# Performance work log

Measured on AMD Instinct MI355X. Metric: run time of the kernel, lower is better.

The kernel has to match this reference:

```python
import jax, jax.numpy as jnp
import numpy as np

# --- SLAYER params (nmnistNet.yaml) ---
THETA = 10.0
TS = 1.0
TAU_REF = 1.0
SCALE_REF = 2.0
T_SAMPLE = 300
B = 8

def _alpha_kernel(tau, mult, t_sample, ts, eps=0.01):
    vals = []
    t = 0.0
    while t < t_sample:
        v = mult * t / tau * np.exp(1.0 - t / tau)
        if abs(v) < eps and t > tau:
            break
        vals.append(v)
        t += ts
    return np.asarray(vals, np.float32)

# refractory kernel: alpha kernel with mult = -scaleRef*theta (slayer._calculateRefKernel)
REF_KERNEL = _alpha_kernel(TAU_REF, -SCALE_REF * THETA, T_SAMPLE, TS)
NREF = REF_KERNEL.shape[0]  # 11 for these params; REF_KERNEL[0] == 0


def spike(u):
    """slayerCuda.getSpikes: per-neuron sequential threshold recurrence over time.
    u: [..., T] membrane potential. On spike at t, REF_KERNEL is accumulated
    into u[t:t+NREF]; spike amplitude is 1/Ts."""
    uT = jnp.moveaxis(u, -1, 0)  # [T, ...]
    refk = jnp.asarray(REF_KERNEL[1:]).reshape((NREF - 1,) + (1,) * (u.ndim - 1))
    buf0 = jnp.zeros((NREF - 1,) + uT.shape[1:], u.dtype)  # pending refractory

    def step(buf, u_t):
        u_mod = u_t + buf[0]
        ev = (u_mod >= THETA).astype(u.dtype)
        buf = jnp.concatenate([buf[1:], jnp.zeros_like(buf[:1])], axis=0) + ev[None] * refk
        return buf, ev / TS

    _, s = jax.lax.scan(step, buf0, uT)
    return jnp.moveaxis(s, 0, -1)


def conv2d_t(x, w, pad):
    """slayer.conv: Conv3d with kernel (k,k,1) == per-timestep 2D conv.
    x: [B,C,H,W,T], w: [O,I,kh,kw]."""
    b, c, h, wd, t = x.shape
    xb = jnp.moveaxis(x, -1, 1).reshape(b * t, c, h, wd)
    y = jax.lax.conv_general_dilated(xb, w, (1, 1), [(pad, pad), (pad, pad)],
                                     dimension_numbers=('NCHW', 'OIHW', 'NCHW'))
    o, ho, wo = y.shape[1], y.shape[2], y.shape[3]
    return jnp.moveaxis(y.reshape(b, t, o, ho, wo), 1, -1)


def sum_pool2(x):
    """slayer.pool(2): fixed-weight (1.1*theta) 2x2/stride-2 sum over H,W per channel."""
    y = jax.lax.reduce_window(x, 0.0, jax.lax.add, (1, 1, 2, 2, 1), (1, 1, 2, 2, 1), 'VALID')
    return 1.1 * THETA * y


def setup_inputs():
    key = jax.random.key(0)
    k0, k1, k2, k3, k4 = jax.random.split(key, 5)
    spikeInput = (jax.random.uniform(k0, (B, 2, 34, 34, T_SAMPLE)) < 0.1).astype(jnp.float32) / TS
    # conv weights: kaiming-uniform bound * 100 (the __init__ scales conv weights by 100)
    w1 = jax.random.uniform(k1, (16, 2, 5, 5), minval=-14.1, maxval=14.1, dtype=jnp.float32)
    w2 = jax.random.uniform(k2, (32, 16, 3, 3), minval=-8.3, maxval=8.3, dtype=jnp.float32)
    w3 = jax.random.uniform(k3, (64, 32, 3, 3), minval=-5.9, maxval=5.9, dtype=jnp.float32)
    wfc = jax.random.uniform(k4, (10, 64, 8, 8), minval=-0.5, maxval=0.5, dtype=jnp.float32)
    return {"spikeInput": spikeInput, "w1": w1, "w2": w2, "w3": w3, "wfc": wfc}


def reference(spikeInput, w1, w2, w3, wfc):
    s1 = spike(conv2d_t(spikeInput, w1, 1))  # [B,16,32,32,T]
    s2 = spike(sum_pool2(s1))                # [B,16,16,16,T]
    s3 = spike(conv2d_t(s2, w2, 1))          # [B,32,16,16,T]
    s4 = spike(sum_pool2(s3))                # [B,32,8,8,T]
    s5 = spike(conv2d_t(s4, w3, 1))          # [B,64,8,8,T]
    # dense((8,8,64),10): Conv3d(64,10,(8,8,1)) == full-spatial contraction
    u = jnp.einsum('bchwt,ochw->bot', s5, wfc)[:, :, None, None, :]
    return spike(u)                          # [B,10,1,1,T]
```

## Files before the change

### kernel.cpp

```cpp
#include <hip/hip_runtime.h>
#include <hip/hip_bf16.h>
#include <cmath>

#define T_SAMPLE 300
#define NCHUNK 75

typedef __attribute__((ext_vector_type(8))) short short8;
typedef __attribute__((ext_vector_type(4))) float f32x4;

struct RefK { float v[10]; };

__device__ __forceinline__ unsigned char spike_step(float u, float* buf, const RefK& rk) {
    const float um = u + buf[0];
    const bool fire = um >= 10.0f;
    const float ev = fire ? 1.0f : 0.0f;
#pragma unroll
    for (int r = 0; r < 9; ++r) buf[r] = fmaf(ev, rk.v[r], buf[r + 1]);
    buf[9] = ev * rk.v[9];
    return fire ? (unsigned char)1 : (unsigned char)0;
}

__device__ __forceinline__ short8 bytes_to_bf16x8(uint2 w8) {
    union { uint4 u; short8 s8; } cv;
    cv.u.x = (w8.x & 0xFFu) * 0x3F80u | ((((w8.x >> 8) & 0xFFu) * 0x3F80u) << 16);
    cv.u.y = ((w8.x >> 16) & 0xFFu) * 0x3F80u | ((((w8.x >> 24) & 0xFFu) * 0x3F80u) << 16);
    cv.u.z = (w8.y & 0xFFu) * 0x3F80u | ((((w8.y >> 8) & 0xFFu) * 0x3F80u) << 16);
    cv.u.w = ((w8.y >> 16) & 0xFFu) * 0x3F80u | ((((w8.y >> 24) & 0xFFu) * 0x3F80u) << 16);
    return cv.s8;
}

__device__ __forceinline__ unsigned short bf16_split_sel(float w, int s) {
    __hip_bfloat16 hb = __float2bfloat16(w);
    const float hf = __bfloat162float(hb);
    __hip_bfloat16 mb = __float2bfloat16(w - hf);
    const float mf = __bfloat162float(mb);
    __hip_bfloat16 lb = __float2bfloat16(w - hf - mf);
    __hip_bfloat16 sel = (s == 0) ? hb : ((s == 1) ? mb : lb);
    return *(unsigned short*)&sel;
}

__global__ __launch_bounds__(256) void transpose_in_k(
    const float* __restrict__ In, unsigned int* __restrict__ X)
{
    __shared__ unsigned int lds[16 * NCHUNK];
    const int blk = blockIdx.x;
    const int tn = threadIdx.x >> 4;
    const int tq = threadIdx.x & 15;
    const size_t n = (size_t)blk * 16 + tn;
#pragma unroll
    for (int p = 0; p < 5; ++p) {
        const int ch = p * 16 + tq;
        if (ch < NCHUNK) {
            const float4 v = *(const float4*)(In + n * T_SAMPLE + ch * 4);
            unsigned int u = (v.x != 0.f ? 1u : 0u) | (v.y != 0.f ? 0x100u : 0u) |
                             (v.z != 0.f ? 0x10000u : 0u) | (v.w != 0.f ? 0x1000000u : 0u);
            lds[tn * NCHUNK + ch] = u;
        }
    }
    __syncthreads();
    for (int idx = threadIdx.x; idx < 16 * NCHUNK; idx += 256) {
        const int ch = idx >> 4, t2 = idx & 15;
        X[(size_t)ch * 18496 + blk * 16 + t2] = lds[t2 * NCHUNK + ch];
    }
}

__global__ __launch_bounds__(256) void prep_w1_k(
    const float* __restrict__ w1, unsigned short* __restrict__ Wr1)
{
    const int g = blockIdx.x * 256 + threadIdx.x;
    const int j = g & 7;
    const int lane = (g >> 3) & 63;
    const int ks = (g >> 9) & 3;
    const int s = g >> 11;
    const int q = lane >> 4;
    const int oc = lane & 15;
    const int kg = ks * 32 + q * 8 + j;
    const int slot = kg >> 2, c = kg & 1;
    const int dy = slot / 6, dx = slot % 6;
    const float w = (dy < 5 && dx < 5) ? w1[((oc * 2 + c) * 5 + dy) * 5 + dx] * 0.5f : 0.f;
    Wr1[g] = bf16_split_sel(w, s);
}

__global__ __launch_bounds__(256) void prep_w3_k(
    const float* __restrict__ w3, unsigned short* __restrict__ Wr)
{
    const int g = blockIdx.x * 256 + threadIdx.x;
    const int j = g & 7;
    const int lane = (g >> 3) & 63;
    const int mt = (g >> 9) & 3;
    const int rest = g >> 11;
    const int ks = rest % 9;
    const int s = rest / 9;
    const int oc = mt * 16 + (lane & 15);
    const int ic = (lane >> 4) * 8 + j;
    Wr[g] = bf16_split_sel(w3[(oc * 32 + ic) * 9 + ks], s);
}

__global__ __launch_bounds__(256) void prep_w2_k(
    const float* __restrict__ w2, unsigned short* __restrict__ Wr2)
{
    const int g = blockIdx.x * 256 + threadIdx.x;
    const int j = g & 7;
    const int lane = (g >> 3) & 63;
    const int mt = (g >> 9) & 1;
    const int rest = g >> 10;
    const int kp = rest % 5;
    const int s = rest / 5;
    const int q = lane >> 4;
    const int oc = mt * 16 + (lane & 15);
    const int tap = kp * 2 + (q >> 1);
    const int ic = (q & 1) * 8 + j;
    const float w = (tap <= 8) ? w2[(oc * 16 + ic) * 9 + tap] : 0.f;
    Wr2[g] = bf16_split_sel(w, s);
}

__global__ __launch_bounds__(256) void conv1_mfma_k(
    const unsigned int* __restrict__ Xu, const unsigned short* __restrict__ Wr1,
    float4* __restrict__ U, int b0, int nbl)
{
    __shared__ __align__(16) unsigned int pad[768];
    const int tc = blockIdx.x;
    const int tile = blockIdx.y;
    const int ty = tile >> 2, tx = tile & 3;
    const int bl = blockIdx.z;
    const int b = b0 + bl;
    const int tid = threadIdx.x;
    const int wv = tid >> 6, lane = tid & 63;
    const int q = lane >> 4, n = lane & 15;
    const int PLANE_U = nbl * 16384;

    for (int i = tid; i < 768; i += 256) pad[i] = 0u;
    __syncthreads();
    const unsigned int* xb = Xu + (size_t)tc * 18496;
    if (tid < 192) {
        const int r = tid >> 4, col = tid & 15;
        const int y = ty * 8 + r - 1, x = tx * 8 + col - 1;
        unsigned int w0 = 0u, w1v = 0u;
        if ((unsigned)y < 34u && (unsigned)x < 34u) {
            w0 = xb[((b * 2 + 0) * 34 + y) * 34 + x];
            w1v = xb[((b * 2 + 1) * 34 + y) * 34 + x];
        }
#pragma unroll
        for (int t = 0; t < 4; ++t) {
            const unsigned int b0b = (w0 >> (8 * t)) & 0xFFu;
            const unsigned int b1b = (w1v >> (8 * t)) & 0xFFu;
            pad[(t * 12 + r) * 16 + col] = b0b | (b1b << 8) | (b0b << 16) | (b1b << 24);
        }
    }
    __syncthreads();

    const int pixel = wv * 16 + n;
    const int py0 = pixel >> 3, px0 = pixel & 7;

    short8 Af[12];
#pragma unroll
    for (int s = 0; s < 3; ++s)
#pragma unroll
        for (int ks = 0; ks < 4; ++ks)
            Af[s * 4 + ks] = *(const short8*)(Wr1 + (((s * 4 + ks) * 64 + lane) * 8));

    f32x4 acc[4];
#pragma unroll
    for (int t = 0; t < 4; ++t) acc[t] = (f32x4){0.f, 0.f, 0.f, 0.f};

#pragma unroll
    for (int ks = 0; ks < 4; ++ks) {
        const int slotA = ks * 8 + q * 2, slotB = slotA + 1;
        const int dyA = slotA / 6, dxA = slotA - dyA * 6;
        const int dyB = slotB / 6, dxB = slotB - dyB * 6;
        const int trA = min(py0 + dyA, 11), trB = min(py0 + dyB, 11);
        const int tcA = px0 + dxA, tcB = px0 + dxB;
#pragma unroll
        for (int t = 0; t < 4; ++t) {
            uint2 w8;
            w8.x = pad[(t * 12 + trA) * 16 + tcA];
            w8.y = pad[(t * 12 + trB) * 16 + tcB];
            const short8 Bf = bytes_to_bf16x8(w8);
#pragma unroll
            for (int s = 0; s < 3; ++s)
                acc[t] = __builtin_amdgcn_mfma_f32_16x16x32_bf16(
                    Af[s * 4 + ks], Bf, acc[t], 0, 0, 0);
        }
    }

    const int y = ty * 8 + py0, x = tx * 8 + px0;
    const size_t ub = (size_t)tc * PLANE_U;
#pragma unroll
    for (int rr = 0; rr < 4; ++rr) {
        const int oc = q * 4 + rr;
        const int nb = (bl * 16 + oc) * 1024 + y * 32 + x;
        U[ub + nb] = make_float4(acc[0][rr], acc[1][rr], acc[2][rr], acc[3][rr]);
    }
}

__global__ __launch_bounds__(256) void conv2_mfma_k(
    const unsigned int* __restrict__ s2u, const unsigned short* __restrict__ Wr2,
    float4* __restrict__ U, int b0, int nbl)
{
    __shared__ __align__(16) unsigned char pad[4 * 18 * 18 * 16];
    const int tc = blockIdx.x;
    const int bl = blockIdx.z;
    const int b = b0 + bl;
    const int tid = threadIdx.x;
    const int wv = tid >> 6, lane = tid & 63;
    const int q = lane >> 4, n = lane & 15;
    const int PLANE_U = nbl * 8192;

    unsigned int* lp = (unsigned int*)pad;
    for (int i = tid; i < 5184; i += 256) lp[i] = 0u;
    __syncthreads();
    const unsigned int* sb = s2u + (size_t)tc * 32768 + b * 4096;
    for (int e = tid; e < 4096; e += 256) {
        const unsigned int v = sb[e];
        const int c = e >> 8, pix = e & 255;
        const int base = (((pix >> 4) + 1) * 18 + ((pix & 15) + 1)) * 16 + c;
        pad[base]         = (unsigned char)(v & 0xFFu);
        pad[5184 + base]  = (unsigned char)((v >> 8) & 0xFFu);
        pad[10368 + base] = (unsigned char)((v >> 16) & 0xFFu);
        pad[15552 + base] = (unsigned char)(v >> 24);
    }
    __syncthreads();

    for (int i = 0; i < 4; ++i) {
        const int r = wv * 4 + i;
        f32x4 acc[2][4];
#pragma unroll
        for (int mt = 0; mt < 2; ++mt)
#pragma unroll
            for (int t = 0; t < 4; ++t) acc[mt][t] = (f32x4){0.f, 0.f, 0.f, 0.f};

        for (int kp = 0; kp < 5; ++kp) {
            short8 Af[6];
#pragma unroll
            for (int s = 0; s < 3; ++s)
#pragma unroll
                for (int mt = 0; mt < 2; ++mt)
                    Af[s * 2 + mt] = *(const short8*)(Wr2 + ((((s * 5 + kp) * 2 + mt) * 64 + lane) * 8));
            int tap = kp * 2 + (q >> 1);
            if (tap > 8) tap = 8;
            const int dy = tap / 3, dx = tap % 3;
#pragma unroll
            for (int t = 0; t < 4; ++t) {
                const int off = ((t * 18 + r + dy) * 18 + (n + dx)) * 16 + (q & 1) * 8;
                const short8 Bf = bytes_to_bf16x8(*(const uint2*)(pad + off));
#pragma unroll
                for (int s = 0; s < 3; ++s)
#pragma unroll
                    for (int mt = 0; mt < 2; ++mt)
                        acc[mt][t] = __builtin_amdgcn_mfma_f32_16x16x32_bf16(
                            Af[s * 2 + mt], Bf, acc[mt][t], 0, 0, 0);
            }
        }

        const size_t ub = (size_t)tc * PLANE_U;
#pragma unroll
        for (int mt = 0; mt < 2; ++mt)
#pragma unroll
            for (int rr = 0; rr < 4; ++rr) {
                const int oc = mt * 16 + q * 4 + rr;
                const int nb = (bl * 32 + oc) * 256 + r * 16 + n;
                U[ub + nb] = make_float4(acc[mt][0][rr], acc[mt][1][rr], acc[mt][2][rr], acc[mt][3][rr]);
            }
    }
}

__global__ __launch_bounds__(256) void conv3_mfma_k(
    const unsigned int* __restrict__ s4u, const unsigned short* __restrict__ Wr,
    float4* __restrict__ U)
{
    __shared__ __align__(16) unsigned char pad[12800];
    const int tc = blockIdx.x;
    const int bl = blockIdx.z;
    const int tid = threadIdx.x;
    const int wv = tid >> 6, lane = tid & 63;
    const int q = lane >> 4, n = lane & 15;

    unsigned int* lp = (unsigned int*)pad;
    for (int i = tid; i < 3200; i += 256) lp[i] = 0u;
    __syncthreads();
    const unsigned int* sb = s4u + (size_t)tc * 16384 + bl * 2048;
    for (int e = tid; e < 2048; e += 256) {
        const unsigned int v = sb[e];
        const int c = e >> 6, pix = e & 63;
        const int base = (((pix >> 3) + 1) * 10 + ((pix & 7) + 1)) * 32 + c;
        pad[base]        = (unsigned char)(v & 0xFFu);
        pad[3200 + base] = (unsigned char)((v >> 8) & 0xFFu);
        pad[6400 + base] = (unsigned char)((v >> 16) & 0xFFu);
        pad[9600 + base] = (unsigned char)(v >> 24);
    }
    __syncthreads();

    const int pixel = wv * 16 + n;
    const int py0 = pixel >> 3, px0 = pixel & 7;

    f32x4 acc[4][4];
#pragma unroll
    for (int mt = 0; mt < 4; ++mt)
#pragma unroll
        for (int t = 0; t < 4; ++t) acc[mt][t] = (f32x4){0.f, 0.f, 0.f, 0.f};

    for (int ks = 0; ks < 9; ++ks) {
        const int dy = ks / 3, dx = ks % 3;
        short8 Af[12];
#pragma unroll
        for (int s = 0; s < 3; ++s)
#pragma unroll
            for (int mt = 0; mt < 4; ++mt)
                Af[s * 4 + mt] = *(const short8*)(Wr + ((((s * 9 + ks) * 4 + mt) * 64 + lane) * 8));
#pragma unroll
        for (int t = 0; t < 4; ++t) {
            const int off = ((t * 10 + py0 + dy) * 10 + (px0 + dx)) * 32 + q * 8;
            const short8 Bf = bytes_to_bf16x8(*(const uint2*)(pad + off));
#pragma unroll
            for (int s = 0; s < 3; ++s)
#pragma unroll
                for (int mt = 0; mt < 4; ++mt)
                    acc[mt][t] = __builtin_amdgcn_mfma_f32_16x16x32_bf16(
                        Af[s * 4 + mt], Bf, acc[mt][t], 0, 0, 0);
        }
    }

    const size_t ub = (size_t)tc * 32768 + (size_t)bl * 4096;
#pragma unroll
    for (int mt = 0; mt < 4; ++mt)
#pragma unroll
        for (int r = 0; r < 4; ++r) {
            const int oc = mt * 16 + q * 4 + r;
            const int nb = oc * 64 + wv * 16 + n;
            U[ub + nb] = make_float4(acc[mt][0][r], acc[mt][1][r], acc[mt][2][r], acc[mt][3][r]);
        }
}

__device__ __forceinline__ void spike_body(
    const float4* __restrict__ U, uchar4* __restrict__ S,
    int nneur, int sstride, int soff, const RefK& rk)
{
    const int n = blockIdx.x * 64 + threadIdx.x;
    const float4* up = U + n;
    uchar4* sp = S + soff + n;
    float buf[10];
#pragma unroll
    for (int r = 0; r < 10; ++r) buf[r] = 0.f;

    float4 ring[8];
#pragma unroll
    for (int r = 0; r < 8; ++r) ring[r] = up[(size_t)r * nneur];

#pragma unroll 8
    for (int ch = 0; ch < 72; ++ch) {
        const float4 cur = ring[ch & 7];
        const int pf = (ch + 8 < NCHUNK) ? ch + 8 : NCHUNK - 1;
        ring[ch & 7] = up[(size_t)pf * nneur];
        uchar4 o;
        o.x = spike_step(cur.x, buf, rk);
        o.y = spike_step(cur.y, buf, rk);
        o.z = spike_step(cur.z, buf, rk);
        o.w = spike_step(cur.w, buf, rk);
        sp[(size_t)ch * sstride] = o;
    }
#pragma unroll
    for (int ch = 72; ch < NCHUNK; ++ch) {
        const float4 cur = ring[ch & 7];
        uchar4 o;
        o.x = spike_step(cur.x, buf, rk);
        o.y = spike_step(cur.y, buf, rk);
        o.z = spike_step(cur.z, buf, rk);
        o.w = spike_step(cur.w, buf, rk);
        sp[(size_t)ch * sstride] = o;
    }
}

__global__ __launch_bounds__(64) void spike1_k(
    const float4* U, uchar4* S, int nneur, int sstride, int soff, RefK rk)
{ spike_body(U, S, nneur, sstride, soff, rk); }

__global__ __launch_bounds__(64) void spike2_k(
    const float4* U, uchar4* S, int nneur, int sstride, int soff, RefK rk)
{ spike_body(U, S, nneur, sstride, soff, rk); }

__global__ __launch_bounds__(64) void spike3_k(
    const float4* U, uchar4* S, int nneur, int sstride, int soff, RefK rk)
{ spike_body(U, S, nneur, sstride, soff, rk); }

__device__ __forceinline__ int bsum4(uint2 r0, uint2 r1, int k) {
    return (int)((r0.x >> (8 * k)) & 0xffu) + (int)((r0.y >> (8 * k)) & 0xffu)
         + (int)((r1.x >> (8 * k)) & 0xffu) + (int)((r1.y >> (8 * k)) & 0xffu);
}

template <int C, int H, int W>
__device__ __forceinline__ void pool_body(
    const uchar4* __restrict__ Sin, uchar4* __restrict__ Sout, const RefK& rk)
{
    constexpr int H2 = H / 2, W2 = W / 2;
    constexpr int SIN = 8 * C * H * W;
    constexpr int SOUT = 8 * C * H2 * W2;
    const int n = blockIdx.x * 64 + threadIdx.x;
    const int x = n % W2;
    const int y = (n / W2) % H2;
    const int c = (n / (W2 * H2)) % C;
    const int b = n / (W2 * H2 * C);
    const int base = (((b * C + c) * H + 2 * y) * W + 2 * x);
    uchar4* q = Sout + n;

    float buf[10];
#pragma unroll
    for (int r = 0; r < 10; ++r) buf[r] = 0.f;

    uint2 r0[8], r1[8];
#pragma unroll
    for (int r = 0; r < 8; ++r) {
        r0[r] = *(const uint2*)(Sin + (size_t)r * SIN + base);
        r1[r] = *(const uint2*)(Sin + (size_t)r * SIN + base + W);
    }

#pragma unroll 8
    for (int ch = 0; ch < 72; ++ch) {
        const uint2 a0 = r0[ch & 7], a1 = r1[ch & 7];
        const int pf = (ch + 8 < NCHUNK) ? ch + 8 : NCHUNK - 1;
        r0[ch & 7] = *(const uint2*)(Sin + (size_t)pf * SIN + base);
        r1[ch & 7] = *(const uint2*)(Sin + (size_t)pf * SIN + base + W);
        uchar4 o;
        o.x = spike_step(11.0f * (float)bsum4(a0, a1, 0), buf, rk);
        o.y = spike_step(11.0f * (float)bsum4(a0, a1, 1), buf, rk);
        o.z = spike_step(11.0f * (float)bsum4(a0, a1, 2), buf, rk);
        o.w = spike_step(11.0f * (float)bsum4(a0, a1, 3), buf, rk);
        q[(size_t)ch * SOUT] = o;
    }
#pragma unroll
    for (int ch = 72; ch < NCHUNK; ++ch) {
        const uint2 a0 = r0[ch & 7], a1 = r1[ch & 7];
        uchar4 o;
        o.x = spike_step(11.0f * (float)bsum4(a0, a1, 0), buf, rk);
        o.y = spike_step(11.0f * (float)bsum4(a0, a1, 1), buf, rk);
        o.z = spike_step(11.0f * (float)bsum4(a0, a1, 2), buf, rk);
        o.w = spike_step(11.0f * (float)bsum4(a0, a1, 3), buf, rk);
        q[(size_t)ch * SOUT] = o;
    }
}

__global__ __launch_bounds__(64) void pool2_k(
    const uchar4* Sin, uchar4* Sout, RefK rk) { pool_body<16, 32, 32>(Sin, Sout, rk); }
__global__ __launch_bounds__(64) void pool4_k(
    const uchar4* Sin, uchar4* Sout, RefK rk) { pool_body<32, 16, 16>(Sin, Sout, rk); }

__global__ __launch_bounds__(64) void dense_k(
    const uchar4* __restrict__ S5, const float* __restrict__ WFC,
    float4* __restrict__ U6)
{
    const int tc = blockIdx.x, o = blockIdx.y, b = blockIdx.z;
    const int lane = threadIdx.x;
    float a0 = 0.f, a1 = 0.f, a2 = 0.f, a3 = 0.f;
    const uchar4* sb = S5 + (size_t)tc * 32768 + b * 4096;
    const float* wb = WFC + o * 4096;
    for (int i = 0; i < 64; ++i) {
        const int site = i * 64 + lane;
        const uchar4 s = sb[site];
        const float w = wb[site];
        a0 = fmaf(w, (float)s.x, a0);
        a1 = fmaf(w, (float)s.y, a1);
        a2 = fmaf(w, (float)s.z, a2);
        a3 = fmaf(w, (float)s.w, a3);
    }
#pragma unroll
    for (int m = 1; m < 64; m <<= 1) {
        a0 += __shfl_xor(a0, m, 64);
        a1 += __shfl_xor(a1, m, 64);
        a2 += __shfl_xor(a2, m, 64);
        a3 += __shfl_xor(a3, m, 64);
    }
    if (lane == 0)
        U6[(size_t)tc * 80 + b * 10 + o] = make_float4(a0, a1, a2, a3);
}

__global__ __launch_bounds__(128) void spike6_k(
    const float4* __restrict__ U6, float* __restrict__ Out, RefK rk)
{
    const int n = threadIdx.x;
    if (n >= 80) return;
    const float4* up = U6 + n;
    float* op = Out + (size_t)n * T_SAMPLE;
    float buf[10];
#pragma unroll
    for (int r = 0; r < 10; ++r) buf[r] = 0.f;

    float4 ring[8];
#pragma unroll
    for (int r = 0; r < 8; ++r) ring[r] = up[(size_t)r * 80];

#pragma unroll 8
    for (int ch = 0; ch < 72; ++ch) {
        const float4 cur = ring[ch & 7];
        const int pf = (ch + 8 < NCHUNK) ? ch + 8 : NCHUNK - 1;
        ring[ch & 7] = up[(size_t)pf * 80];
        float4 o;
        o.x = (float)spike_step(cur.x, buf, rk);
        o.y = (float)spike_step(cur.y, buf, rk);
        o.z = (float)spike_step(cur.z, buf, rk);
        o.w = (float)spike_step(cur.w, buf, rk);
        *(float4*)(op + ch * 4) = o;
    }
#pragma unroll
    for (int ch = 72; ch < NCHUNK; ++ch) {
        const float4 cur = ring[ch & 7];
        float4 o;
        o.x = (float)spike_step(cur.x, buf, rk);
        o.y = (float)spike_step(cur.y, buf, rk);
        o.z = (float)spike_step(cur.z, buf, rk);
        o.w = (float)spike_step(cur.w, buf, rk);
        *(float4*)(op + ch * 4) = o;
    }
}

extern "C" void kernel_launch(void* const* d_in, const int* in_sizes, int n_in,
                              void* d_out, int out_size, void* d_ws, size_t ws_size,
                              hipStream_t stream)
{
    const float* spikeIn = (const float*)d_in[0];
    const float* w1 = (const float*)d_in[1];
    const float* w2 = (const float*)d_in[2];
    const float* w3 = (const float*)d_in[3];
    const float* wfc = (const float*)d_in[4];
    float* out = (float*)d_out;

    RefK rk;
    for (int t = 1; t <= 10; ++t)
        rk.v[t - 1] = (float)(-20.0 * (double)t * std::exp(1.0 - (double)t));

    const size_t A_BYTES = 39321600;
    const size_t B_BYTES = 9830400;
    const size_t U6_BYTES = 96000;
    const size_t U_HUGE = 157286400, U_BIG = 78643200, U_SMALL = 39321600;
    const size_t TAIL = A_BYTES + B_BYTES + U6_BYTES;
    const bool huge = ws_size >= U_HUGE + TAIL;
    const bool big = ws_size >= U_BIG + TAIL;
    const size_t U_BYTES = huge ? U_HUGE : (big ? U_BIG : U_SMALL);

    char* ws = (char*)d_ws;
    float4* U = (float4*)ws;
    uchar4* A = (uchar4*)(ws + U_BYTES);
    uchar4* Bb = (uchar4*)(ws + U_BYTES + A_BYTES);
    float4* U6 = (float4*)(ws + U_BYTES + A_BYTES + B_BYTES);
    unsigned short* Wr = (unsigned short*)(ws + U_BYTES + 20971520);
    unsigned short* Wr2 = (unsigned short*)(ws + U_BYTES + 20971520 + 131072);
    unsigned short* Wr1 = (unsigned short*)(ws + U_BYTES + A_BYTES + 5570560);

    uchar4* X = Bb;
    uchar4* s1 = A;
    uchar4* s2 = Bb;
    uchar4* s3 = A;
    uchar4* s4 = Bb;
    uchar4* s5 = A;

    transpose_in_k<<<18496 / 16, 256, 0, stream>>>(spikeIn, (unsigned int*)X);
    prep_w1_k<<<24, 256, 0, stream>>>(w1, Wr1);

    const int nbl1 = huge ? 8 : (big ? 4 : 2);
    for (int b0 = 0; b0 < 8; b0 += nbl1) {
        dim3 g1(NCHUNK, 16, nbl1);
        conv1_mfma_k<<<g1, 256, 0, stream>>>((const unsigned int*)X, Wr1, U, b0, nbl1);
        const int nn = nbl1 * 16384;
        spike1_k<<<nn / 64, 64, 0, stream>>>(U, s1, nn, 131072, b0 * 16384, rk);
    }
    pool2_k<<<32768 / 64, 64, 0, stream>>>(s1, s2, rk);
    prep_w2_k<<<60, 256, 0, stream>>>(w2, Wr2);
    prep_w3_k<<<216, 256, 0, stream>>>(w3, Wr);
    const int nbl2 = (huge || big) ? 8 : 4;
    for (int b0 = 0; b0 < 8; b0 += nbl2) {
        dim3 g2(NCHUNK, 1, nbl2);
        conv2_mfma_k<<<g2, 256, 0, stream>>>((const unsigned int*)s2, Wr2, U, b0, nbl2);
        const int nn = nbl2 * 8192;
        spike2_k<<<nn / 64, 64, 0, stream>>>(U, s3, nn, 65536, b0 * 8192, rk);
    }
    pool4_k<<<16384 / 64, 64, 0, stream>>>(s3, s4, rk);
    {
        dim3 g3(NCHUNK, 1, 8);
        conv3_mfma_k<<<g3, 256, 0, stream>>>((const unsigned int*)s4, Wr, U);
        spike3_k<<<32768 / 64, 64, 0, stream>>>(U, s5, 32768, 32768, 0, rk);
    }
    dim3 g6(NCHUNK, 10, 8);
    dense_k<<<g6, 64, 0, stream>>>(s5, wfc, U6);
    spike6_k<<<1, 128, 0, stream>>>(U6, out, rk);
}
```

Baseline: 287.8 us.

## Fuse conv1 with spike recurrence, iterating time chunks inside one kernel

Replaces the conv1 kernel and its separate spike pass with a fused kernel. Each 64-thread block owns a 2x8 pixel tile for one batch and loops over all 75 time chunks, carrying refractory state in registers and prefetching the next chunk into registers. This removes the large float membrane-potential buffer round trip through global memory. A new repack kernel pre-expands input bytes to bf16 pairs. The cost is a grid of only 512 small blocks running a serial time loop, which lowers parallelism and latency hiding.

```diff
diff --git a/kernel.cpp b/kernel.cpp
--- a/kernel.cpp
+++ b/kernel.cpp
@@ -61,6 +61,25 @@
     for (int idx = threadIdx.x; idx < 16 * NCHUNK; idx += 256) {
         const int ch = idx >> 4, t2 = idx & 15;
         X[(size_t)ch * 18496 + blk * 16 + t2] = lds[t2 * NCHUNK + ch];
+    }
+}
+
+__global__ __launch_bounds__(256) void repack1_k(
+    const unsigned int* __restrict__ X, uint2* __restrict__ X2)
+{
+    const int g = blockIdx.x * 256 + threadIdx.x;
+    if (g >= 693600) return;
+    const int yx = g % 1156;
+    const int rest = g / 1156;
+    const int b = rest & 7;
+    const int ch = rest >> 3;
+    const unsigned int w0 = X[(size_t)ch * 18496 + (b * 2 + 0) * 1156 + yx];
+    const unsigned int w1 = X[(size_t)ch * 18496 + (b * 2 + 1) * 1156 + yx];
+#pragma unroll
+    for (int t = 0; t < 4; ++t) {
+        const unsigned int u = ((w0 >> (8 * t)) & 0xFFu) * 0x3F80u
+                             | ((((w1 >> (8 * t)) & 0xFFu) * 0x3F80u) << 16);
+        X2[(((size_t)ch * 4 + t) * 8 + b) * 1156 + yx] = make_uint2(u, u);
     }
 }
 
@@ -114,43 +133,17 @@
     Wr2[g] = bf16_split_sel(w, s);
 }
 
-__global__ __launch_bounds__(256) void conv1_mfma_k(
-    const unsigned int* __restrict__ Xu, const unsigned short* __restrict__ Wr1,
-    float4* __restrict__ U, int b0, int nbl)
-{
-    __shared__ __align__(16) unsigned int pad[768];
-    const int tc = blockIdx.x;
-    const int tile = blockIdx.y;
-    const int ty = tile >> 2, tx = tile & 3;
-    const int bl = blockIdx.z;
-    const int b = b0 + bl;
-    const int tid = threadIdx.x;
-    const int wv = tid >> 6, lane = tid & 63;
+__global__ __launch_bounds__(64) void conv1s_mfma_k(
+    const uint2* __restrict__ X2, const unsigned short* __restrict__ Wr1,
+    uchar4* __restrict__ S1, RefK rk)
+{
+    __shared__ __align__(16) uint2 sh[288];
+    const int pg = blockIdx.x;
+    const int b = blockIdx.y;
+    const int ty = pg >> 2, tx = pg & 3;
+    const int lane = threadIdx.x;
     const int q = lane >> 4, n = lane & 15;
-    const int PLANE_U = nbl * 16384;
-
-    for (int i = tid; i < 768; i += 256) pad[i] = 0u;
-    __syncthreads();
-    const unsigned int* xb = Xu + (size_t)tc * 18496;
-    if (tid < 192) {
-        const int r = tid >> 4, col = tid & 15;
-        const int y = ty * 8 + r - 1, x = tx * 8 + col - 1;
-        unsigned int w0 = 0u, w1v = 0u;
-        if ((unsigned)y < 34u && (unsigned)x < 34u) {
-            w0 = xb[((b * 2 + 0) * 34 + y) * 34 + x];
-            w1v = xb[((b * 2 + 1) * 34 + y) * 34 + x];
-        }
-#pragma unroll
-        for (int t = 0; t < 4; ++t) {
-            const unsigned int b0b = (w0 >> (8 * t)) & 0xFFu;
-            const unsigned int b1b = (w1v >> (8 * t)) & 0xFFu;
-            pad[(t * 12 + r) * 16 + col] = b0b | (b1b << 8) | (b0b << 16) | (b1b << 24);
-        }
-    }
-    __syncthreads();
-
-    const int pixel = wv * 16 + n;
-    const int py0 = pixel >> 3, px0 = pixel & 7;
+    const int py0 = n >> 3, px0 = n & 7;
 
     short8 Af[12];
 #pragma unroll
@@ -159,37 +152,83 @@
         for (int ks = 0; ks < 4; ++ks)
             Af[s * 4 + ks] = *(const short8*)(Wr1 + (((s * 4 + ks) * 64 + lane) * 8));
 
-    f32x4 acc[4];
-#pragma unroll
-    for (int t = 0; t < 4; ++t) acc[t] = (f32x4){0.f, 0.f, 0.f, 0.f};
-
+    int lofs[5]; int gofs[5]; bool gval[5];
+#pragma unroll
+    for (int i = 0; i < 5; ++i) {
+        const int e = i * 64 + lane;
+        if (e < 288) {
+            const int t = e / 72, s = e - t * 72;
+            const int r = s / 12, cc = s - r * 12;
+            const int gy = ty * 2 - 1 + r, gx = tx * 8 - 1 + cc;
+            gval[i] = ((unsigned)gy < 34u) && ((unsigned)gx < 34u);
+            lofs[i] = e;
+            gofs[i] = (t * 8 + b) * 1156 + gy * 34 + gx;
+        } else { gval[i] = false; lofs[i] = -1; gofs[i] = 0; }
+    }
+
+    uint2 pf[5];
+#pragma unroll
+    for (int i = 0; i < 5; ++i) pf[i] = make_uint2(0u, 0u);
+#pragma unroll
+    for (int i = 0; i < 5; ++i) if (gval[i]) pf[i] = X2[gofs[i]];
+
+    int offA[4], offB[4];
 #pragma unroll
     for (int ks = 0; ks < 4; ++ks) {
-        const int slotA = ks * 8 + q * 2, slotB = slotA + 1;
-        const int dyA = slotA / 6, dxA = slotA - dyA * 6;
-        const int dyB = slotB / 6, dxB = slotB - dyB * 6;
-        const int trA = min(py0 + dyA, 11), trB = min(py0 + dyB, 11);
-        const int tcA = px0 + dxA, tcB = px0 + dxB;
-#pragma unroll
-        for (int t = 0; t < 4; ++t) {
-            uint2 w8;
-            w8.x = pad[(t * 12 + trA) * 16 + tcA];
-            w8.y = pad[(t * 12 + trB) * 16 + tcB];
-            const short8 Bf = bytes_to_bf16x8(w8);
-#pragma unroll
-            for (int s = 0; s < 3; ++s)
-                acc[t] = __builtin_amdgcn_mfma_f32_16x16x32_bf16(
-                    Af[s * 4 + ks], Bf, acc[t], 0, 0, 0);
+        const int sA = ks * 8 + q * 2, sB = sA + 1;
+        const int dyA = sA / 6, dxA = sA - dyA * 6;
+        const int dyB = sB / 6, dxB = sB - dyB * 6;
+        offA[ks] = min(py0 + dyA, 5) * 12 + min(px0 + dxA, 11);
+        offB[ks] = min(py0 + dyB, 5) * 12 + min(px0 + dxB, 11);
+    }
+
+    float buf[4][10];
+#pragma unroll
+    for (int rr = 0; rr < 4; ++rr)
+#pragma unroll
+        for (int r = 0; r < 10; ++r) buf[rr][r] = 0.f;
+
+    const int nb0 = (b * 16 + q * 4) * 1024 + (ty * 2 + py0) * 32 + tx * 8 + px0;
+
+    for (int ch = 0; ch < NCHUNK; ++ch) {
+        __syncthreads();
+#pragma unroll
+        for (int i = 0; i < 5; ++i) if (lofs[i] >= 0) sh[lofs[i]] = pf[i];
+        __syncthreads();
+
+        if (ch + 1 < NCHUNK) {
+            const uint2* src = X2 + (size_t)(ch + 1) * 36992;
+#pragma unroll
+            for (int i = 0; i < 5; ++i) if (gval[i]) pf[i] = src[gofs[i]];
         }
-    }
-
-    const int y = ty * 8 + py0, x = tx * 8 + px0;
-    const size_t ub = (size_t)tc * PLANE_U;
-#pragma unroll
-    for (int rr = 0; rr < 4; ++rr) {
-        const int oc = q * 4 + rr;
-        const int nb = (bl * 16 + oc) * 1024 + y * 32 + x;
-        U[ub + nb] = make_float4(acc[0][rr], acc[1][rr], acc[2][rr], acc[3][rr]);
+
+        f32x4 acc[4];
+#pragma unroll
+        for (int t = 0; t < 4; ++t) acc[t] = (f32x4){0.f, 0.f, 0.f, 0.f};
+
+#pragma unroll
+        for (int ks = 0; ks < 4; ++ks)
+#pragma unroll
+            for (int t = 0; t < 4; ++t) {
+                const uint2 a = sh[offA[ks] + t * 72];
+                const uint2 bq = sh[offB[ks] + t * 72];
+                union { uint4 u; short8 s8; } cv;
+                cv.u.x = a.x; cv.u.y = a.y; cv.u.z = bq.x; cv.u.w = bq.y;
+#pragma unroll
+                for (int s = 0; s < 3; ++s)
+                    acc[t] = __builtin_amdgcn_mfma_f32_16x16x32_bf16(
+                        Af[s * 4 + ks], cv.s8, acc[t], 0, 0, 0);
+            }
+
+#pragma unroll
+        for (int rr = 0; rr < 4; ++rr) {
+            uchar4 o;
+            o.x = spike_step(acc[0][rr], buf[rr], rk);
+            o.y = spike_step(acc[1][rr], buf[rr], rk);
+            o.z = spike_step(acc[2][rr], buf[rr], rk);
+            o.w = spike_step(acc[3][rr], buf[rr], rk);
+            S1[(size_t)ch * 131072 + nb0 + rr * 1024] = o;
+        }
     }
 }
 
@@ -369,10 +408,6 @@
         sp[(size_t)ch * sstride] = o;
     }
 }
-
-__global__ __launch_bounds__(64) void spike1_k(
-    const float4* U, uchar4* S, int nneur, int sstride, int soff, RefK rk)
-{ spike_body(U, S, nneur, sstride, soff, rk); }
 
 __global__ __launch_bounds__(64) void spike2_k(
     const float4* U, uchar4* S, int nneur, int sstride, int soff, RefK rk)
@@ -543,6 +578,7 @@
     unsigned short* Wr = (unsigned short*)(ws + U_BYTES + 20971520);
     unsigned short* Wr2 = (unsigned short*)(ws + U_BYTES + 20971520 + 131072);
     unsigned short* Wr1 = (unsigned short*)(ws + U_BYTES + A_BYTES + 5570560);
+    uint2* X2 = (uint2*)ws;
 
     uchar4* X = Bb;
     uchar4* s1 = A;
@@ -553,13 +589,11 @@
 
     transpose_in_k<<<18496 / 16, 256, 0, stream>>>(spikeIn, (unsigned int*)X);
     prep_w1_k<<<24, 256, 0, stream>>>(w1, Wr1);
-
-    const int nbl1 = huge ? 8 : (big ? 4 : 2);
-    for (int b0 = 0; b0 < 8; b0 += nbl1) {
-        dim3 g1(NCHUNK, 16, nbl1);
-        conv1_mfma_k<<<g1, 256, 0, stream>>>((const unsigned int*)X, Wr1, U, b0, nbl1);
-        const int nn = nbl1 * 16384;
-        spike1_k<<<nn / 64, 64, 0, stream>>>(U, s1, nn, 131072, b0 * 16384, rk);
+    repack1_k<<<2710, 256, 0, stream>>>((const unsigned int*)X, X2);
+
+    {
+        dim3 g1(64, 8);
+        conv1s_mfma_k<<<g1, 64, 0, stream>>>(X2, Wr1, s1, rk);
     }
     pool2_k<<<32768 / 64, 64, 0, stream>>>(s1, s2, rk);
     prep_w2_k<<<60, 256, 0, stream>>>(w2, Wr2);
```

New measurement: 394.3 us. +37.0%, slower.

## Split conv1/conv2 and spike stages into time phases with carried refractory state

Applied to the files above, without the earlier changes.

Rather than batching conv+spike over subsets of the batch, the conv1 and conv2 stages are now split along time into phases (5 of 15 chunks, 3 of 25 chunks), with all 8 batches per launch. The spike kernel saves its refractory buffer to a state array between phases and reloads it at the start of the next. This keeps the membrane-potential buffer smaller and more cache-resident, and gives every spike launch the full neuron count for better parallelism. The cost is extra state reads and writes and more kernel launches. The workspace-size branching is also removed.

```diff
diff --git a/kernel.cpp b/kernel.cpp
--- a/kernel.cpp
+++ b/kernel.cpp
@@ -116,22 +116,20 @@
 
 __global__ __launch_bounds__(256) void conv1_mfma_k(
     const unsigned int* __restrict__ Xu, const unsigned short* __restrict__ Wr1,
-    float4* __restrict__ U, int b0, int nbl)
+    float4* __restrict__ U, int c0)
 {
     __shared__ __align__(16) unsigned int pad[768];
-    const int tc = blockIdx.x;
+    const int tcl = blockIdx.x;
     const int tile = blockIdx.y;
     const int ty = tile >> 2, tx = tile & 3;
-    const int bl = blockIdx.z;
-    const int b = b0 + bl;
+    const int b = blockIdx.z;
     const int tid = threadIdx.x;
     const int wv = tid >> 6, lane = tid & 63;
     const int q = lane >> 4, n = lane & 15;
-    const int PLANE_U = nbl * 16384;
 
     for (int i = tid; i < 768; i += 256) pad[i] = 0u;
     __syncthreads();
-    const unsigned int* xb = Xu + (size_t)tc * 18496;
+    const unsigned int* xb = Xu + (size_t)(c0 + tcl) * 18496;
     if (tid < 192) {
         const int r = tid >> 4, col = tid & 15;
         const int y = ty * 8 + r - 1, x = tx * 8 + col - 1;
@@ -184,32 +182,30 @@
     }
 
     const int y = ty * 8 + py0, x = tx * 8 + px0;
-    const size_t ub = (size_t)tc * PLANE_U;
+    const size_t ub = (size_t)tcl * 131072;
 #pragma unroll
     for (int rr = 0; rr < 4; ++rr) {
         const int oc = q * 4 + rr;
-        const int nb = (bl * 16 + oc) * 1024 + y * 32 + x;
+        const int nb = (b * 16 + oc) * 1024 + y * 32 + x;
         U[ub + nb] = make_float4(acc[0][rr], acc[1][rr], acc[2][rr], acc[3][rr]);
     }
 }
 
 __global__ __launch_bounds__(256) void conv2_mfma_k(
     const unsigned int* __restrict__ s2u, const unsigned short* __restrict__ Wr2,
-    float4* __restrict__ U, int b0, int nbl)
+    float4* __restrict__ U, int c0)
 {
     __shared__ __align__(16) unsigned char pad[4 * 18 * 18 * 16];
-    const int tc = blockIdx.x;
-    const int bl = blockIdx.z;
-    const int b = b0 + bl;
+    const int tcl = blockIdx.x;
+    const int b = blockIdx.z;
     const int tid = threadIdx.x;
     const int wv = tid >> 6, lane = tid & 63;
     const int q = lane >> 4, n = lane & 15;
-    const int PLANE_U = nbl * 8192;
 
     unsigned int* lp = (unsigned int*)pad;
     for (int i = tid; i < 5184; i += 256) lp[i] = 0u;
     __syncthreads();
-    const unsigned int* sb = s2u + (size_t)tc * 32768 + b * 4096;
+    const unsigned int* sb = s2u + (size_t)(c0 + tcl) * 32768 + b * 4096;
     for (int e = tid; e < 4096; e += 256) {
         const unsigned int v = sb[e];
         const int c = e >> 8, pix = e & 255;
@@ -252,13 +248,13 @@
             }
         }
 
-        const size_t ub = (size_t)tc * PLANE_U;
+        const size_t ub = (size_t)tcl * 65536;
 #pragma unroll
         for (int mt = 0; mt < 2; ++mt)
 #pragma unroll
             for (int rr = 0; rr < 4; ++rr) {
                 const int oc = mt * 16 + q * 4 + rr;
-                const int nb = (bl * 32 + oc) * 256 + r * 16 + n;
+                const int nb = (b * 32 + oc) * 256 + r * 16 + n;
                 U[ub + nb] = make_float4(acc[mt][0][rr], acc[mt][1][rr], acc[mt][2][rr], acc[mt][3][rr]);
             }
     }
@@ -331,56 +327,55 @@
         }
 }
 
-__device__ __forceinline__ void spike_body(
+template <int TB>
+__global__ __launch_bounds__(64) void spike_phase_k(
     const float4* __restrict__ U, uchar4* __restrict__ S,
-    int nneur, int sstride, int soff, const RefK& rk)
+    float* __restrict__ St, int nneur, int c0, RefK rk)
 {
     const int n = blockIdx.x * 64 + threadIdx.x;
     const float4* up = U + n;
-    uchar4* sp = S + soff + n;
+    uchar4* sp = S + (size_t)c0 * nneur + n;
+
     float buf[10];
-#pragma unroll
-    for (int r = 0; r < 10; ++r) buf[r] = 0.f;
+    if (c0 == 0) {
+#pragma unroll
+        for (int r = 0; r < 10; ++r) buf[r] = 0.f;
+    } else {
+#pragma unroll
+        for (int r = 0; r < 10; ++r) buf[r] = St[(size_t)r * nneur + n];
+    }
 
     float4 ring[8];
 #pragma unroll
     for (int r = 0; r < 8; ++r) ring[r] = up[(size_t)r * nneur];
 
 #pragma unroll 8
-    for (int ch = 0; ch < 72; ++ch) {
+    for (int ch = 0; ch < TB - 8; ++ch) {
         const float4 cur = ring[ch & 7];
-        const int pf = (ch + 8 < NCHUNK) ? ch + 8 : NCHUNK - 1;
-        ring[ch & 7] = up[(size_t)pf * nneur];
+        ring[ch & 7] = up[(size_t)(ch + 8) * nneur];
         uchar4 o;
         o.x = spike_step(cur.x, buf, rk);
         o.y = spike_step(cur.y, buf, rk);
         o.z = spike_step(cur.z, buf, rk);
         o.w = spike_step(cur.w, buf, rk);
-        sp[(size_t)ch * sstride] = o;
-    }
-#pragma unroll
-    for (int ch = 72; ch < NCHUNK; ++ch) {
+        sp[(size_t)ch * nneur] = o;
+    }
+#pragma unroll
+    for (int ch = TB - 8; ch < TB; ++ch) {
         const float4 cur = ring[ch & 7];
         uchar4 o;
         o.x = spike_step(cur.x, buf, rk);
         o.y = spike_step(cur.y, buf, rk);
         o.z = spike_step(cur.z, buf, rk);
         o.w = spike_step(cur.w, buf, rk);
-        sp[(size_t)ch * sstride] = o;
-    }
-}
-
-__global__ __launch_bounds__(64) void spike1_k(
-    const float4* U, uchar4* S, int nneur, int sstride, int soff, RefK rk)
-{ spike_body(U, S, nneur, sstride, soff, rk); }
-
-__global__ __launch_bounds__(64) void spike2_k(
-    const float4* U, uchar4* S, int nneur, int sstride, int soff, RefK rk)
-{ spike_body(U, S, nneur, sstride, soff, rk); }
-
-__global__ __launch_bounds__(64) void spike3_k(
-    const float4* U, uchar4* S, int nneur, int sstride, int soff, RefK rk)
-{ spike_body(U, S, nneur, sstride, soff, rk); }
+        sp[(size_t)ch * nneur] = o;
+    }
+
+    if (c0 + TB < NCHUNK) {
+#pragma unroll
+        for (int r = 0; r < 10; ++r) St[(size_t)r * nneur + n] = buf[r];
+    }
+}
 
 __device__ __forceinline__ int bsum4(uint2 r0, uint2 r1, int k) {
     return (int)((r0.x >> (8 * k)) & 0xffu) + (int)((r0.y >> (8 * k)) & 0xffu)
@@ -528,12 +523,7 @@
 
     const size_t A_BYTES = 39321600;
     const size_t B_BYTES = 9830400;
-    const size_t U6_BYTES = 96000;
-    const size_t U_HUGE = 157286400, U_BIG = 78643200, U_SMALL = 39321600;
-    const size_t TAIL = A_BYTES + B_BYTES + U6_BYTES;
-    const bool huge = ws_size >= U_HUGE + TAIL;
-    const bool big = ws_size >= U_BIG + TAIL;
-    const size_t U_BYTES = huge ? U_HUGE : (big ? U_BIG : U_SMALL);
+    const size_t U_BYTES = 39321600;
 
     char* ws = (char*)d_ws;
     float4* U = (float4*)ws;
@@ -543,6 +533,8 @@
     unsigned short* Wr = (unsigned short*)(ws + U_BYTES + 20971520);
     unsigned short* Wr2 = (unsigned short*)(ws + U_BYTES + 20971520 + 131072);
     unsigned short* Wr1 = (unsigned short*)(ws + U_BYTES + A_BYTES + 5570560);
+    float* St1 = (float*)(ws + 31457280);
+    float* St2 = (float*)(ws + 26214400);
 
     uchar4* X = Bb;
     uchar4* s1 = A;
@@ -554,28 +546,26 @@
     transpose_in_k<<<18496 / 16, 256, 0, stream>>>(spikeIn, (unsigned int*)X);
     prep_w1_k<<<24, 256, 0, stream>>>(w1, Wr1);
 
-    const int nbl1 = huge ? 8 : (big ? 4 : 2);
-    for (int b0 = 0; b0 < 8; b0 += nbl1) {
-        dim3 g1(NCHUNK, 16, nbl1);
-        conv1_mfma_k<<<g1, 256, 0, stream>>>((const unsigned int*)X, Wr1, U, b0, nbl1);
-        const int nn = nbl1 * 16384;
-        spike1_k<<<nn / 64, 64, 0, stream>>>(U, s1, nn, 131072, b0 * 16384, rk);
+    for (int p = 0; p < 5; ++p) {
+        const int c0 = p * 15;
+        dim3 g1(15, 16, 8);
+        conv1_mfma_k<<<g1, 256, 0, stream>>>((const unsigned int*)X, Wr1, U, c0);
+        spike_phase_k<15><<<131072 / 64, 64, 0, stream>>>(U, s1, St1, 131072, c0, rk);
     }
     pool2_k<<<32768 / 64, 64, 0, stream>>>(s1, s2, rk);
     prep_w2_k<<<60, 256, 0, stream>>>(w2, Wr2);
     prep_w3_k<<<216, 256, 0, stream>>>(w3, Wr);
-    const int nbl2 = (huge || big) ? 8 : 4;
-    for (int b0 = 0; b0 < 8; b0 += nbl2) {
-        dim3 g2(NCHUNK, 1, nbl2);
-        conv2_mfma_k<<<g2, 256, 0, stream>>>((const unsigned int*)s2, Wr2, U, b0, nbl2);
-        const int nn = nbl2 * 8192;
-        spike2_k<<<nn / 64, 64, 0, stream>>>(U, s3, nn, 65536, b0 * 8192, rk);
+    for (int p = 0; p < 3; ++p) {
+        const int c0 = p * 25;
+        dim3 g2(25, 1, 8);
+        conv2_mfma_k<<<g2, 256, 0, stream>>>((const unsigned int*)s2, Wr2, U, c0);
+        spike_phase_k<25><<<65536 / 64, 64, 0, stream>>>(U, s3, St2, 65536, c0, rk);
     }
     pool4_k<<<16384 / 64, 64, 0, stream>>>(s3, s4, rk);
     {
         dim3 g3(NCHUNK, 1, 8);
         conv3_mfma_k<<<g3, 256, 0, stream>>>((const unsigned int*)s4, Wr, U);
-        spike3_k<<<32768 / 64, 64, 0, stream>>>(U, s5, 32768, 32768, 0, rk);
+        spike_phase_k<75><<<32768 / 64, 64, 0, stream>>>(U, s5, (float*)0, 32768, 0, rk);
     }
     dim3 g6(NCHUNK, 10, 8);
     dense_k<<<g6, 64, 0, stream>>>(s5, wfc, U6);
```

New measurement: 390.7 us. 35.8% more time.
